# Optimization experiments

Measured on AMD Instinct MI355X. Metric: run time of the kernel, lower is better.

## Reference

```python
import jax, jax.numpy as jnp
import numpy as np

B, S, D = 4, 4096, 1024
BS = 8            # block size
N = D // BS       # num blocks = 128
K = 8             # gate levels


def _cayley_real_block(A_r, A_i):
    # A_r, A_i: [M, BS, BS]. Solve (I+A) U = (I-A) in the real 2BSx2BS isomorphism.
    M = A_r.shape[0]
    eye = jnp.eye(BS, dtype=A_r.dtype)[None]
    IpA_r = eye + A_r
    ImA_r = eye - A_r
    LHS = jnp.concatenate([
        jnp.concatenate([IpA_r, -A_i], axis=-1),
        jnp.concatenate([A_i, IpA_r], axis=-1)], axis=-2)  # [M,2BS,2BS]
    RHS = jnp.concatenate([
        jnp.concatenate([ImA_r, A_i], axis=-1),
        jnp.concatenate([-A_i, ImA_r], axis=-1)], axis=-2)
    U_rb = jnp.linalg.solve(LHS, RHS)
    return U_rb[:, :BS, :BS], U_rb[:, BS:, :BS]


def setup_inputs() -> dict:
    key = jax.random.key(0)
    k1, k2, k3, k4, k5 = jax.random.split(key, 5)
    x_real = jax.random.normal(k1, (B, S, D), dtype=jnp.float32)
    x_imag = jax.random.normal(k2, (B, S, D), dtype=jnp.float32)
    A_real = jax.random.normal(k3, (N, BS, BS), dtype=jnp.float32) * 0.02
    A_imag = jax.random.normal(k4, (N, BS, BS), dtype=jnp.float32) * 0.02
    W_gate = jax.random.normal(k5, (2 * D, D), dtype=jnp.float32) * (1.0 / np.sqrt(2 * D))
    b_gate = jnp.zeros((D,), dtype=jnp.float32)
    return {"x_real": x_real, "x_imag": x_imag, "A_real": A_real,
            "A_imag": A_imag, "W_gate": W_gate, "b_gate": b_gate}


def reference(x_real, x_imag, A_real, A_imag, W_gate, b_gate):
    # Gate: sigmoid(Linear([re, im]) * 1.7015)
    x_cat = jnp.concatenate([x_real, x_imag], axis=-1)          # [B,S,2D]
    gate = jax.nn.sigmoid((x_cat @ W_gate + b_gate) * 1.7015)    # [B,S,D]
    g_cont = gate.reshape(B, S, N, BS).mean(axis=-1)             # [B,S,N]
    level_idx = jnp.clip(jnp.round(g_cont * (K - 1)).astype(jnp.int32), 0, K - 1)
    g_levels = jnp.linspace(0.0, 1.0, K, dtype=x_real.dtype)
    g_quant = g_levels[level_idx]                                # [B,S,N]
    g_st = g_cont + jax.lax.stop_gradient(g_quant - g_cont)      # straight-through

    # Anti-Hermitian generator: skew-sym real part, sym imag part
    A_r = (A_real - jnp.swapaxes(A_real, -2, -1)) * 0.5          # [N,BS,BS]
    A_i = (A_imag + jnp.swapaxes(A_imag, -2, -1)) * 0.5

    # K*N scaled generators -> Cayley unitaries
    g_scale = g_levels[:, None, None, None]                      # [K,1,1,1]
    gA_r = (g_scale * A_r[None]).reshape(K * N, BS, BS)
    gA_i = (g_scale * A_i[None]).reshape(K * N, BS, BS)
    U_r_all, U_i_all = _cayley_real_block(gA_r, gA_i)
    U_r_all = U_r_all.reshape(K, N, BS, BS)
    U_i_all = U_i_all.reshape(K, N, BS, BS)

    # Gather per-token, per-block unitary: [B,S,N,BS,BS]
    blk = jnp.arange(N)
    U_r = U_r_all[level_idx, blk]
    U_i = U_i_all[level_idx, blk]

    xr = x_real.reshape(B, S, N, BS)
    xi = x_imag.reshape(B, S, N, BS)
    Ux_r = jnp.einsum('bsnoi,bsni->bsno', U_r, xr) - jnp.einsum('bsnoi,bsni->bsno', U_i, xi)
    Ux_i = jnp.einsum('bsnoi,bsni->bsno', U_r, xi) + jnp.einsum('bsnoi,bsni->bsno', U_i, xr)

    scale = (g_st / (g_quant + 1e-7))[..., None]                 # [B,S,N,1]
    out_r = xr + scale * (Ux_r - xr)
    out_i = xi + scale * (Ux_i - xi)
    return jax.lax.complex(out_r.reshape(B, S, D), out_i.reshape(B, S, D))
```

## Files before the change

### kernel.cpp

```cpp
#include <hip/hip_runtime.h>
#include <hip/hip_bf16.h>
#include <math.h>

#define BB 4
#define SS 4096
#define DD 1024
#define NN 128
#define KLV 8
#define MM (BB*SS)
#define NST 64

typedef short bf16x8 __attribute__((ext_vector_type(8)));
typedef float f32x4 __attribute__((ext_vector_type(4)));

__device__ unsigned short g_U16[KLV * NN * 128];
__device__ unsigned char g_levels[MM * NN];
__device__ unsigned short g_WTs[(size_t)NST * 2 * 4 * 1024 * 8];

__device__ __forceinline__ unsigned int bf16_bits(float f) {
    union { float f; unsigned int u; } v;
    v.f = f;
    unsigned int lsb = (v.u >> 16) & 1u;
    return (v.u + 0x7FFFu + lsb) >> 16;
}
__device__ __forceinline__ float bfbits2f(unsigned int b) {
    union { unsigned int u; float f; } v;
    v.u = b << 16;
    return v.f;
}

#define WT_BLOCKS (64 * 32)
__global__ __launch_bounds__(256)
void prep_kernel(const float* __restrict__ W,
                 const float* __restrict__ A_real,
                 const float* __restrict__ A_imag)
{
    __shared__ __align__(16) float sh[33 * 32];
    int blk = blockIdx.x;
    int t = threadIdx.x;

    if (blk < WT_BLOCKS) {
        float (*tile)[33] = (float(*)[33])sh;
        int bk = (blk >> 5) * 32;
        int bn = (blk & 31) * 32;

        int kk = t >> 3;
        int nn4 = (t & 7) * 4;
        float4 v = *(const float4*)&W[(size_t)(bk + kk) * DD + bn + nn4];
        tile[kk][nn4 + 0] = v.x; tile[kk][nn4 + 1] = v.y;
        tile[kk][nn4 + 2] = v.z; tile[kk][nn4 + 3] = v.w;
        __syncthreads();

        int n2 = t >> 3;
        int k4i = (t & 7) * 4;
        unsigned int hi[4], lo[4];
        #pragma unroll
        for (int q = 0; q < 4; ++q) {
            float f = tile[k4i + q][n2];
            hi[q] = bf16_bits(f);
            lo[q] = bf16_bits(f - bfbits2f(hi[q]));
        }
        int st = bk >> 5;
        int kgrp = (k4i >> 3) & 3;
        int kin = k4i & 7;
        int n = bn + n2;
        size_t bh = ((size_t)((st * 2 + 0) * 4 + kgrp) * 1024 + n) * 8 + kin;
        size_t bl = ((size_t)((st * 2 + 1) * 4 + kgrp) * 1024 + n) * 8 + kin;
        *(uint2*)&g_WTs[bh] = make_uint2(hi[0] | (hi[1] << 16), hi[2] | (hi[3] << 16));
        *(uint2*)&g_WTs[bl] = make_uint2(lo[0] | (lo[1] << 16), lo[2] | (lo[3] << 16));
        return;
    }
    blk -= WT_BLOCKS;

    {
        float (*M)[34] = (float(*)[34])sh;
        int L = blk >> 7;
        int n = blk & 127;
        float g = (float)L * (1.0f / 7.0f);

        int i = t >> 4;
        int j = t & 15;

        const float* Ar = A_real + n * 64;
        const float* Ai = A_imag + n * 64;
        int bi = i >> 3;
        int ii = i & 7, jj = j & 7;

        float ar = (Ar[ii * 8 + jj] - Ar[jj * 8 + ii]) * 0.5f * g;
        float ai = (Ai[ii * 8 + jj] + Ai[jj * 8 + ii]) * 0.5f * g;
        float eye = (ii == jj) ? 1.0f : 0.0f;

        int bj = j >> 3;
        float lhs, rhs;
        if (bi == bj) { lhs = eye + ar; rhs = eye - ar; }
        else if (bi == 0) { lhs = -ai; rhs = ai; }
        else { lhs = ai; rhs = -ai; }

        M[i][j] = lhs;
        M[i][16 + j] = rhs;
        __syncthreads();

        for (int k = 0; k < 16; ++k) {
            float f = M[i][k] / M[k][k];
            __syncthreads();
            if (i != k) {
                M[i][j]      -= f * M[k][j];
                M[i][16 + j] -= f * M[k][16 + j];
            }
            __syncthreads();
        }

        float x = M[i][16 + j] / M[i][i];
        if (j < 8) {
            g_U16[(size_t)blk * 128 + bi * 64 + ii * 8 + j] =
                (unsigned short)bf16_bits(x);
        }
    }
}

__global__ __launch_bounds__(256, 2)
void gate_v4(const float* __restrict__ xr, const float* __restrict__ xi,
             const float* __restrict__ bias)
{
    __shared__ __align__(16) unsigned short lds[8192];

    const int tid = threadIdx.x;
    const int bid = blockIdx.x;
    const int xcd = bid & 7;
    const int grp = bid >> 3;
    const int mt = xcd * 16 + (grp >> 2);
    const int nt = grp & 3;
    const int bm = mt * 128, bn = nt * 256;

    const int lane = tid & 63;
    const int wc = tid >> 6;
    const int r16 = lane & 15, sgrp = lane >> 4;

    const int arow = tid >> 1;
    const int kb = (tid & 1) * 2;

    f32x4 acc[8][4];
    #pragma unroll
    for (int a = 0; a < 8; ++a)
        #pragma unroll
        for (int b = 0; b < 4; ++b) {
            f32x4 z = {0.0f, 0.0f, 0.0f, 0.0f};
            acc[a][b] = z;
        }

    #define LOADX(dst, s)                                                         \
    {                                                                             \
        int s_ = (s) > 63 ? 63 : (s);                                             \
        int k0_ = s_ * 32;                                                        \
        const float* src_ = (k0_ < 1024) ? xr : xi;                               \
        const float* p_ = src_ + (size_t)(bm + arow) * DD + (k0_ & 1023)          \
                          + (tid & 1) * 16;                                       \
        (dst)[0] = *(const float4*)(p_);                                          \
        (dst)[1] = *(const float4*)(p_ + 4);                                      \
        (dst)[2] = *(const float4*)(p_ + 8);                                      \
        (dst)[3] = *(const float4*)(p_ + 12);                                     \
    }

    #define WRITEA(fv, bb)                                                        \
    {                                                                             \
        float ff_[16] = {(fv)[0].x, (fv)[0].y, (fv)[0].z, (fv)[0].w,              \
                         (fv)[1].x, (fv)[1].y, (fv)[1].z, (fv)[1].w,              \
                         (fv)[2].x, (fv)[2].y, (fv)[2].z, (fv)[2].w,              \
                         (fv)[3].x, (fv)[3].y, (fv)[3].z, (fv)[3].w};             \
        unsigned int h_[16];                                                      \
        _Pragma("unroll")                                                         \
        for (int q = 0; q < 16; ++q) h_[q] = bf16_bits(ff_[q]);                   \
        _Pragma("unroll")                                                         \
        for (int b2 = 0; b2 < 2; ++b2) {                                          \
            int o_ = ((kb + b2) * 128 + arow) * 8;                                \
            *(uint4*)&lds[(bb) + o_] = make_uint4(                                \
                h_[b2*8+0] | (h_[b2*8+1] << 16), h_[b2*8+2] | (h_[b2*8+3] << 16), \
                h_[b2*8+4] | (h_[b2*8+5] << 16), h_[b2*8+6] | (h_[b2*8+7] << 16));\
        }                                                                         \
    }

    #define RA(bb, mi) (*(const bf16x8*)&lds[(bb) + \
        (sgrp * 128 + (mi) * 16 + r16) * 8])
    #define BW(s, plane, ni) (*(const bf16x8*)&g_WTs[ \
        ((size_t)((((s) > 63 ? 63 : (s)) * 2 + (plane)) * 4 + sgrp) * 1024 + \
         (bn + wc * 64 + (ni) * 16 + r16)) * 8])

    float4 fst[4], ftmp[4];
    LOADX(fst, 0);
    WRITEA(fst, 0);
    LOADX(fst, 1);
    asm volatile("s_waitcnt lgkmcnt(0)" ::: "memory");
    __builtin_amdgcn_s_barrier();

    for (int st = 0; st < NST; ++st) {
        const int bcur = (st & 1) * 4096;
        const int bnxt = bcur ^ 4096;

        bf16x8 whf[4], wlf[4], ahi[8];
        #pragma unroll
        for (int ni = 0; ni < 4; ++ni) whf[ni] = BW(st, 0, ni);
        #pragma unroll
        for (int ni = 0; ni < 4; ++ni) wlf[ni] = BW(st, 1, ni);

        WRITEA(fst, bnxt);
        LOADX(ftmp, st + 2);

        #pragma unroll
        for (int mi = 0; mi < 8; ++mi) ahi[mi] = RA(bcur, mi);

        __builtin_amdgcn_s_setprio(1);
        #pragma unroll
        for (int mi = 0; mi < 8; ++mi)
            #pragma unroll
            for (int ni = 0; ni < 4; ++ni)
                acc[mi][ni] = __builtin_amdgcn_mfma_f32_16x16x32_bf16(
                    ahi[mi], whf[ni], acc[mi][ni], 0, 0, 0);
        __builtin_amdgcn_s_setprio(0);
        __builtin_amdgcn_s_setprio(1);
        #pragma unroll
        for (int mi = 0; mi < 8; ++mi)
            #pragma unroll
            for (int ni = 0; ni < 4; ++ni)
                acc[mi][ni] = __builtin_amdgcn_mfma_f32_16x16x32_bf16(
                    ahi[mi], wlf[ni], acc[mi][ni], 0, 0, 0);
        __builtin_amdgcn_s_setprio(0);

        asm volatile("s_waitcnt lgkmcnt(0)" ::: "memory");
        __builtin_amdgcn_s_barrier();
        #pragma unroll
        for (int q = 0; q < 4; ++q) fst[q] = ftmp[q];
    }
    #undef LOADX
    #undef WRITEA
    #undef RA
    #undef BW

    #pragma unroll
    for (int mi = 0; mi < 8; ++mi) {
        #pragma unroll
        for (int ni = 0; ni < 4; ++ni) {
            int n = bn + wc * 64 + ni * 16 + r16;
            float bb = bias[n];
            #pragma unroll
            for (int r = 0; r < 4; ++r) {
                float z = (acc[mi][ni][r] + bb) * 1.7015f;
                float s = 1.0f / (1.0f + expf(-z));
                s += __shfl_xor(s, 1);
                s += __shfl_xor(s, 2);
                s += __shfl_xor(s, 4);
                if ((lane & 7) == 0) {
                    float gcont = s * 0.125f;
                    int lvl = (int)rintf(gcont * 7.0f);
                    lvl = min(7, max(0, lvl));
                    int m = bm + mi * 16 + sgrp * 4 + r;
                    g_levels[(size_t)m * NN + (n >> 3)] = (unsigned char)lvl;
                }
            }
        }
    }
}

__global__ __launch_bounds__(256)
void apply_kernel(const float* __restrict__ xr,
                  const float* __restrict__ xi,
                  unsigned short* __restrict__ out)
{
    int t = blockIdx.x * 256 + threadIdx.x;
    int bs = t >> 7;
    int n = t & 127;

    int L = g_levels[t];
    const unsigned short* Up = g_U16 + (size_t)(L * NN + n) * 128;
    const float* xrp = xr + (size_t)bs * DD + n * 8;
    const float* xip = xi + (size_t)bs * DD + n * 8;

    float4 r0 = *(const float4*)xrp;
    float4 r1 = *(const float4*)(xrp + 4);
    float4 i0 = *(const float4*)xip;
    float4 i1 = *(const float4*)(xip + 4);
    float xrv[8] = {r0.x, r0.y, r0.z, r0.w, r1.x, r1.y, r1.z, r1.w};
    float xiv[8] = {i0.x, i0.y, i0.z, i0.w, i1.x, i1.y, i1.z, i1.w};

    float gq = (float)L * (1.0f / 7.0f);
    float scale = gq / (gq + 1e-7f);

    unsigned int pk[8];
    #pragma unroll
    for (int oo = 0; oo < 8; ++oo) {
        uint4 uw = *(const uint4*)&Up[oo * 8];
        uint4 vw = *(const uint4*)&Up[64 + oo * 8];
        unsigned int uwa[4] = {uw.x, uw.y, uw.z, uw.w};
        unsigned int vwa[4] = {vw.x, vw.y, vw.z, vw.w};
        float ur[8], ui[8];
        #pragma unroll
        for (int q = 0; q < 4; ++q) {
            ur[2*q]   = bfbits2f(uwa[q] & 0xFFFFu);
            ur[2*q+1] = bfbits2f(uwa[q] >> 16);
            ui[2*q]   = bfbits2f(vwa[q] & 0xFFFFu);
            ui[2*q+1] = bfbits2f(vwa[q] >> 16);
        }
        float uxr = 0.0f, uxi = 0.0f;
        #pragma unroll
        for (int q = 0; q < 8; ++q) {
            uxr += ur[q] * xrv[q] - ui[q] * xiv[q];
            uxi += ur[q] * xiv[q] + ui[q] * xrv[q];
        }
        float outr = xrv[oo] + scale * (uxr - xrv[oo]);
        float outi = xiv[oo] + scale * (uxi - xiv[oo]);
        pk[oo] = bf16_bits(outi) | (bf16_bits(outr) << 16);
    }

    unsigned int* ob = (unsigned int*)(out + 2 * ((size_t)bs * DD + (size_t)n * 8));
    *(uint4*)&ob[0] = make_uint4(pk[0], pk[1], pk[2], pk[3]);
    *(uint4*)&ob[4] = make_uint4(pk[4], pk[5], pk[6], pk[7]);
}

extern "C" void kernel_launch(void* const* d_in, const int* in_sizes, int n_in,
                              void* d_out, int out_size, void* d_ws, size_t ws_size,
                              hipStream_t stream) {
    (void)in_sizes; (void)n_in; (void)out_size; (void)d_ws; (void)ws_size;
    const float* x_real = (const float*)d_in[0];
    const float* x_imag = (const float*)d_in[1];
    const float* A_real = (const float*)d_in[2];
    const float* A_imag = (const float*)d_in[3];
    const float* W_gate = (const float*)d_in[4];
    const float* b_gate = (const float*)d_in[5];
    unsigned short* out = (unsigned short*)d_out;

    hipLaunchKernelGGL(prep_kernel, dim3(WT_BLOCKS + KLV * NN), dim3(256),
                       0, stream, W_gate, A_real, A_imag);
    hipLaunchKernelGGL(gate_v4, dim3(512), dim3(256), 0, stream,
                       x_real, x_imag, b_gate);
    hipLaunchKernelGGL(apply_kernel, dim3((MM * NN) / 256), dim3(256), 0, stream,
                       x_real, x_imag, out);
}
```

Measured before the change: 230.1 us.

## Pre-convert activations to bf16 and load GEMM operands directly from global

Result: slower. 296.2 us (+28.7%).

```diff
diff --git a/kernel.cpp b/kernel.cpp
--- a/kernel.cpp
+++ b/kernel.cpp
@@ -15,6 +15,7 @@
 
 __device__ unsigned short g_U16[KLV * NN * 128];
 __device__ unsigned char g_levels[MM * NN];
+__device__ unsigned short g_XH[(size_t)MM * 2048];
 __device__ unsigned short g_WTs[(size_t)NST * 2 * 4 * 1024 * 8];
 
 __device__ __forceinline__ unsigned int bf16_bits(float f) {
@@ -31,13 +32,32 @@
 
 #define WT_BLOCKS (64 * 32)
 __global__ __launch_bounds__(256)
-void prep_kernel(const float* __restrict__ W,
+void prep_kernel(const float* __restrict__ xr, const float* __restrict__ xi,
+                 const float* __restrict__ W,
                  const float* __restrict__ A_real,
                  const float* __restrict__ A_imag)
 {
     __shared__ __align__(16) float sh[33 * 32];
     int blk = blockIdx.x;
     int t = threadIdx.x;
+
+    if (blk < MM) {
+        int m = blk;
+        const float* src = (t < 128) ? xr : xi;
+        int off = (t & 127) * 8;
+        const float* p = src + (size_t)m * DD + off;
+        float4 v0 = *(const float4*)p;
+        float4 v1 = *(const float4*)(p + 4);
+        float f[8] = {v0.x, v0.y, v0.z, v0.w, v1.x, v1.y, v1.z, v1.w};
+        unsigned int h[8];
+        #pragma unroll
+        for (int q = 0; q < 8; ++q) h[q] = bf16_bits(f[q]);
+        *(uint4*)&g_XH[(size_t)m * 2048 + t * 8] = make_uint4(
+            h[0] | (h[1] << 16), h[2] | (h[3] << 16),
+            h[4] | (h[5] << 16), h[6] | (h[7] << 16));
+        return;
+    }
+    blk -= MM;
 
     if (blk < WT_BLOCKS) {
         float (*tile)[33] = (float(*)[33])sh;
@@ -119,11 +139,8 @@
 }
 
 __global__ __launch_bounds__(256, 2)
-void gate_v4(const float* __restrict__ xr, const float* __restrict__ xi,
-             const float* __restrict__ bias)
+void gate_v8(const float* __restrict__ bias)
 {
-    __shared__ __align__(16) unsigned short lds[8192];
-
     const int tid = threadIdx.x;
     const int bid = blockIdx.x;
     const int xcd = bid & 7;
@@ -136,9 +153,6 @@
     const int wc = tid >> 6;
     const int r16 = lane & 15, sgrp = lane >> 4;
 
-    const int arow = tid >> 1;
-    const int kb = (tid & 1) * 2;
-
     f32x4 acc[8][4];
     #pragma unroll
     for (int a = 0; a < 8; ++a)
@@ -148,65 +162,22 @@
             acc[a][b] = z;
         }
 
-    #define LOADX(dst, s)                                                         \
-    {                                                                             \
-        int s_ = (s) > 63 ? 63 : (s);                                             \
-        int k0_ = s_ * 32;                                                        \
-        const float* src_ = (k0_ < 1024) ? xr : xi;                               \
-        const float* p_ = src_ + (size_t)(bm + arow) * DD + (k0_ & 1023)          \
-                          + (tid & 1) * 16;                                       \
-        (dst)[0] = *(const float4*)(p_);                                          \
-        (dst)[1] = *(const float4*)(p_ + 4);                                      \
-        (dst)[2] = *(const float4*)(p_ + 8);                                      \
-        (dst)[3] = *(const float4*)(p_ + 12);                                     \
-    }
-
-    #define WRITEA(fv, bb)                                                        \
-    {                                                                             \
-        float ff_[16] = {(fv)[0].x, (fv)[0].y, (fv)[0].z, (fv)[0].w,              \
-                         (fv)[1].x, (fv)[1].y, (fv)[1].z, (fv)[1].w,              \
-                         (fv)[2].x, (fv)[2].y, (fv)[2].z, (fv)[2].w,              \
-                         (fv)[3].x, (fv)[3].y, (fv)[3].z, (fv)[3].w};             \
-        unsigned int h_[16];                                                      \
-        _Pragma("unroll")                                                         \
-        for (int q = 0; q < 16; ++q) h_[q] = bf16_bits(ff_[q]);                   \
-        _Pragma("unroll")                                                         \
-        for (int b2 = 0; b2 < 2; ++b2) {                                          \
-            int o_ = ((kb + b2) * 128 + arow) * 8;                                \
-            *(uint4*)&lds[(bb) + o_] = make_uint4(                                \
-                h_[b2*8+0] | (h_[b2*8+1] << 16), h_[b2*8+2] | (h_[b2*8+3] << 16), \
-                h_[b2*8+4] | (h_[b2*8+5] << 16), h_[b2*8+6] | (h_[b2*8+7] << 16));\
-        }                                                                         \
-    }
-
-    #define RA(bb, mi) (*(const bf16x8*)&lds[(bb) + \
-        (sgrp * 128 + (mi) * 16 + r16) * 8])
-    #define BW(s, plane, ni) (*(const bf16x8*)&g_WTs[ \
-        ((size_t)((((s) > 63 ? 63 : (s)) * 2 + (plane)) * 4 + sgrp) * 1024 + \
-         (bn + wc * 64 + (ni) * 16 + r16)) * 8])
-
-    float4 fst[4], ftmp[4];
-    LOADX(fst, 0);
-    WRITEA(fst, 0);
-    LOADX(fst, 1);
-    asm volatile("s_waitcnt lgkmcnt(0)" ::: "memory");
-    __builtin_amdgcn_s_barrier();
+    const unsigned short* Abase = g_XH + (size_t)(bm + r16) * 2048 + sgrp * 8;
+    const unsigned short* Bbase = g_WTs + ((size_t)sgrp * 1024 +
+                                           (bn + wc * 64 + r16)) * 8;
 
     for (int st = 0; st < NST; ++st) {
-        const int bcur = (st & 1) * 4096;
-        const int bnxt = bcur ^ 4096;
-
-        bf16x8 whf[4], wlf[4], ahi[8];
-        #pragma unroll
-        for (int ni = 0; ni < 4; ++ni) whf[ni] = BW(st, 0, ni);
-        #pragma unroll
-        for (int ni = 0; ni < 4; ++ni) wlf[ni] = BW(st, 1, ni);
-
-        WRITEA(fst, bnxt);
-        LOADX(ftmp, st + 2);
-
-        #pragma unroll
-        for (int mi = 0; mi < 8; ++mi) ahi[mi] = RA(bcur, mi);
+        bf16x8 whf[4], wlf[4], ahf[8];
+        #pragma unroll
+        for (int ni = 0; ni < 4; ++ni) {
+            whf[ni] = *(const bf16x8*)(Bbase +
+                ((size_t)(st * 2 + 0) * 4 * 1024 + ni * 16) * 8);
+            wlf[ni] = *(const bf16x8*)(Bbase +
+                ((size_t)(st * 2 + 1) * 4 * 1024 + ni * 16) * 8);
+        }
+        #pragma unroll
+        for (int mi = 0; mi < 8; ++mi)
+            ahf[mi] = *(const bf16x8*)(Abase + (size_t)mi * 16 * 2048 + st * 32);
 
         __builtin_amdgcn_s_setprio(1);
         #pragma unroll
@@ -214,7 +185,7 @@
             #pragma unroll
             for (int ni = 0; ni < 4; ++ni)
                 acc[mi][ni] = __builtin_amdgcn_mfma_f32_16x16x32_bf16(
-                    ahi[mi], whf[ni], acc[mi][ni], 0, 0, 0);
+                    ahf[mi], whf[ni], acc[mi][ni], 0, 0, 0);
         __builtin_amdgcn_s_setprio(0);
         __builtin_amdgcn_s_setprio(1);
         #pragma unroll
@@ -222,18 +193,9 @@
             #pragma unroll
             for (int ni = 0; ni < 4; ++ni)
                 acc[mi][ni] = __builtin_amdgcn_mfma_f32_16x16x32_bf16(
-                    ahi[mi], wlf[ni], acc[mi][ni], 0, 0, 0);
+                    ahf[mi], wlf[ni], acc[mi][ni], 0, 0, 0);
         __builtin_amdgcn_s_setprio(0);
-
-        asm volatile("s_waitcnt lgkmcnt(0)" ::: "memory");
-        __builtin_amdgcn_s_barrier();
-        #pragma unroll
-        for (int q = 0; q < 4; ++q) fst[q] = ftmp[q];
-    }
-    #undef LOADX
-    #undef WRITEA
-    #undef RA
-    #undef BW
+    }
 
     #pragma unroll
     for (int mi = 0; mi < 8; ++mi) {
@@ -327,10 +289,9 @@
     const float* b_gate = (const float*)d_in[5];
     unsigned short* out = (unsigned short*)d_out;
 
-    hipLaunchKernelGGL(prep_kernel, dim3(WT_BLOCKS + KLV * NN), dim3(256),
-                       0, stream, W_gate, A_real, A_imag);
-    hipLaunchKernelGGL(gate_v4, dim3(512), dim3(256), 0, stream,
-                       x_real, x_imag, b_gate);
+    hipLaunchKernelGGL(prep_kernel, dim3(MM + WT_BLOCKS + KLV * NN), dim3(256),
+                       0, stream, x_real, x_imag, W_gate, A_real, A_imag);
+    hipLaunchKernelGGL(gate_v8, dim3(512), dim3(256), 0, stream, b_gate);
     hipLaunchKernelGGL(apply_kernel, dim3((MM * NN) / 256), dim3(256), 0, stream,
                        x_real, x_imag, out);
 }
```

## Fuse unitary apply into gate GEMM epilogue via LDS-staged levels

Applied to the files above, without the earlier changes.

Result: faster. 219.8 us (-4.5%).

```diff
diff --git a/kernel.cpp b/kernel.cpp
--- a/kernel.cpp
+++ b/kernel.cpp
@@ -14,7 +14,6 @@
 typedef float f32x4 __attribute__((ext_vector_type(4)));
 
 __device__ unsigned short g_U16[KLV * NN * 128];
-__device__ unsigned char g_levels[MM * NN];
 __device__ unsigned short g_WTs[(size_t)NST * 2 * 4 * 1024 * 8];
 
 __device__ __forceinline__ unsigned int bf16_bits(float f) {
@@ -119,8 +118,9 @@
 }
 
 __global__ __launch_bounds__(256, 2)
-void gate_v4(const float* __restrict__ xr, const float* __restrict__ xi,
-             const float* __restrict__ bias)
+void gate_fused(const float* __restrict__ xr, const float* __restrict__ xi,
+                const float* __restrict__ bias,
+                unsigned short* __restrict__ out)
 {
     __shared__ __align__(16) unsigned short lds[8192];
 
@@ -167,15 +167,16 @@
                          (fv)[1].x, (fv)[1].y, (fv)[1].z, (fv)[1].w,              \
                          (fv)[2].x, (fv)[2].y, (fv)[2].z, (fv)[2].w,              \
                          (fv)[3].x, (fv)[3].y, (fv)[3].z, (fv)[3].w};             \
-        unsigned int h_[16];                                                      \
+        unsigned int w_[8];                                                       \
         _Pragma("unroll")                                                         \
-        for (int q = 0; q < 16; ++q) h_[q] = bf16_bits(ff_[q]);                   \
+        for (int q = 0; q < 8; ++q)                                               \
+            asm("v_cvt_pk_bf16_f32 %0, %1, %2"                                    \
+                : "=v"(w_[q]) : "v"(ff_[2*q]), "v"(ff_[2*q+1]));                  \
         _Pragma("unroll")                                                         \
         for (int b2 = 0; b2 < 2; ++b2) {                                          \
             int o_ = ((kb + b2) * 128 + arow) * 8;                                \
             *(uint4*)&lds[(bb) + o_] = make_uint4(                                \
-                h_[b2*8+0] | (h_[b2*8+1] << 16), h_[b2*8+2] | (h_[b2*8+3] << 16), \
-                h_[b2*8+4] | (h_[b2*8+5] << 16), h_[b2*8+6] | (h_[b2*8+7] << 16));\
+                w_[b2*4+0], w_[b2*4+1], w_[b2*4+2], w_[b2*4+3]);                  \
         }                                                                         \
     }
 
@@ -235,12 +236,13 @@
     #undef RA
     #undef BW
 
+    unsigned char* lvl_lds = (unsigned char*)lds;
     #pragma unroll
     for (int mi = 0; mi < 8; ++mi) {
         #pragma unroll
         for (int ni = 0; ni < 4; ++ni) {
-            int n = bn + wc * 64 + ni * 16 + r16;
-            float bb = bias[n];
+            int nl = wc * 64 + ni * 16 + r16;
+            float bb = bias[bn + nl];
             #pragma unroll
             for (int r = 0; r < 4; ++r) {
                 float z = (acc[mi][ni][r] + bb) * 1.7015f;
@@ -252,67 +254,69 @@
                     float gcont = s * 0.125f;
                     int lvl = (int)rintf(gcont * 7.0f);
                     lvl = min(7, max(0, lvl));
-                    int m = bm + mi * 16 + sgrp * 4 + r;
-                    g_levels[(size_t)m * NN + (n >> 3)] = (unsigned char)lvl;
+                    int row = mi * 16 + sgrp * 4 + r;
+                    lvl_lds[row * 32 + (nl >> 3)] = (unsigned char)lvl;
                 }
             }
         }
     }
-}
-
-__global__ __launch_bounds__(256)
-void apply_kernel(const float* __restrict__ xr,
-                  const float* __restrict__ xi,
-                  unsigned short* __restrict__ out)
-{
-    int t = blockIdx.x * 256 + threadIdx.x;
-    int bs = t >> 7;
-    int n = t & 127;
-
-    int L = g_levels[t];
-    const unsigned short* Up = g_U16 + (size_t)(L * NN + n) * 128;
-    const float* xrp = xr + (size_t)bs * DD + n * 8;
-    const float* xip = xi + (size_t)bs * DD + n * 8;
-
-    float4 r0 = *(const float4*)xrp;
-    float4 r1 = *(const float4*)(xrp + 4);
-    float4 i0 = *(const float4*)xip;
-    float4 i1 = *(const float4*)(xip + 4);
-    float xrv[8] = {r0.x, r0.y, r0.z, r0.w, r1.x, r1.y, r1.z, r1.w};
-    float xiv[8] = {i0.x, i0.y, i0.z, i0.w, i1.x, i1.y, i1.z, i1.w};
-
-    float gq = (float)L * (1.0f / 7.0f);
-    float scale = gq / (gq + 1e-7f);
-
-    unsigned int pk[8];
-    #pragma unroll
-    for (int oo = 0; oo < 8; ++oo) {
-        uint4 uw = *(const uint4*)&Up[oo * 8];
-        uint4 vw = *(const uint4*)&Up[64 + oo * 8];
-        unsigned int uwa[4] = {uw.x, uw.y, uw.z, uw.w};
-        unsigned int vwa[4] = {vw.x, vw.y, vw.z, vw.w};
-        float ur[8], ui[8];
-        #pragma unroll
-        for (int q = 0; q < 4; ++q) {
-            ur[2*q]   = bfbits2f(uwa[q] & 0xFFFFu);
-            ur[2*q+1] = bfbits2f(uwa[q] >> 16);
-            ui[2*q]   = bfbits2f(vwa[q] & 0xFFFFu);
-            ui[2*q+1] = bfbits2f(vwa[q] >> 16);
-        }
-        float uxr = 0.0f, uxi = 0.0f;
-        #pragma unroll
-        for (int q = 0; q < 8; ++q) {
-            uxr += ur[q] * xrv[q] - ui[q] * xiv[q];
-            uxi += ur[q] * xiv[q] + ui[q] * xrv[q];
-        }
-        float outr = xrv[oo] + scale * (uxr - xrv[oo]);
-        float outi = xiv[oo] + scale * (uxi - xiv[oo]);
-        pk[oo] = bf16_bits(outi) | (bf16_bits(outr) << 16);
-    }
-
-    unsigned int* ob = (unsigned int*)(out + 2 * ((size_t)bs * DD + (size_t)n * 8));
-    *(uint4*)&ob[0] = make_uint4(pk[0], pk[1], pk[2], pk[3]);
-    *(uint4*)&ob[4] = make_uint4(pk[4], pk[5], pk[6], pk[7]);
+    __syncthreads();
+
+    const int nb0 = bn >> 3;
+    #pragma unroll 2
+    for (int it = 0; it < 16; ++it) {
+        int p = it * 256 + tid;
+        int row = p >> 5;
+        int nbi = p & 31;
+        int m = bm + row;
+        int nb = nb0 + nbi;
+        int n0 = nb * 8;
+
+        int L = lvl_lds[row * 32 + nbi];
+        const unsigned short* Up = g_U16 + (size_t)(L * NN + nb) * 128;
+        const float* xrp = xr + (size_t)m * DD + n0;
+        const float* xip = xi + (size_t)m * DD + n0;
+
+        float4 r0 = *(const float4*)xrp;
+        float4 r1 = *(const float4*)(xrp + 4);
+        float4 i0 = *(const float4*)xip;
+        float4 i1 = *(const float4*)(xip + 4);
+        float xrv[8] = {r0.x, r0.y, r0.z, r0.w, r1.x, r1.y, r1.z, r1.w};
+        float xiv[8] = {i0.x, i0.y, i0.z, i0.w, i1.x, i1.y, i1.z, i1.w};
+
+        float gq = (float)L * (1.0f / 7.0f);
+        float scale = gq / (gq + 1e-7f);
+
+        unsigned int pk[8];
+        #pragma unroll
+        for (int oo = 0; oo < 8; ++oo) {
+            uint4 uw = *(const uint4*)&Up[oo * 8];
+            uint4 vw = *(const uint4*)&Up[64 + oo * 8];
+            unsigned int uwa[4] = {uw.x, uw.y, uw.z, uw.w};
+            unsigned int vwa[4] = {vw.x, vw.y, vw.z, vw.w};
+            float ur[8], ui[8];
+            #pragma unroll
+            for (int q = 0; q < 4; ++q) {
+                ur[2*q]   = bfbits2f(uwa[q] & 0xFFFFu);
+                ur[2*q+1] = bfbits2f(uwa[q] >> 16);
+                ui[2*q]   = bfbits2f(vwa[q] & 0xFFFFu);
+                ui[2*q+1] = bfbits2f(vwa[q] >> 16);
+            }
+            float uxr = 0.0f, uxi = 0.0f;
+            #pragma unroll
+            for (int q = 0; q < 8; ++q) {
+                uxr += ur[q] * xrv[q] - ui[q] * xiv[q];
+                uxi += ur[q] * xiv[q] + ui[q] * xrv[q];
+            }
+            float outr = xrv[oo] + scale * (uxr - xrv[oo]);
+            float outi = xiv[oo] + scale * (uxi - xiv[oo]);
+            pk[oo] = bf16_bits(outi) | (bf16_bits(outr) << 16);
+        }
+
+        unsigned int* ob = (unsigned int*)(out + 2 * ((size_t)m * DD + n0));
+        *(uint4*)&ob[0] = make_uint4(pk[0], pk[1], pk[2], pk[3]);
+        *(uint4*)&ob[4] = make_uint4(pk[4], pk[5], pk[6], pk[7]);
+    }
 }
 
 extern "C" void kernel_launch(void* const* d_in, const int* in_sizes, int n_in,
@@ -329,8 +333,6 @@
 
     hipLaunchKernelGGL(prep_kernel, dim3(WT_BLOCKS + KLV * NN), dim3(256),
                        0, stream, W_gate, A_real, A_imag);
-    hipLaunchKernelGGL(gate_v4, dim3(512), dim3(256), 0, stream,
-                       x_real, x_imag, b_gate);
-    hipLaunchKernelGGL(apply_kernel, dim3((MM * NN) / 256), dim3(256), 0, stream,
-                       x_real, x_imag, out);
-}
+    hipLaunchKernelGGL(gate_fused, dim3(512), dim3(256), 0, stream,
+                       x_real, x_imag, b_gate, out);
+}
```
